# Performance work log

Measured on AMD Instinct MI355X. Metric: run time of the kernel, lower is better.

## Reference

```python
import jax, jax.numpy as jnp
import numpy as np

UNITS = 32
BACKBONE = 64

def lecun_tanh(x):
    return 1.7159 * jnp.tanh(0.666 * x)

def setup_inputs() -> dict:
    key = jax.random.key(0)
    ks = jax.random.split(key, 6)
    B, C, T, H, W = 4, 16, 32, 64, 64
    scale_b = 1.0 / np.sqrt(C + UNITS)
    scale_h = 1.0 / np.sqrt(BACKBONE)
    return {
        "x": jax.random.normal(ks[0], (B, C, T, H, W), jnp.float32),
        "Wb": jax.random.normal(ks[1], (BACKBONE, C + UNITS), jnp.float32) * scale_b,
        "bb": jnp.zeros((BACKBONE,), jnp.float32),
        "Wff1": jax.random.normal(ks[2], (UNITS, BACKBONE), jnp.float32) * scale_h,
        "bff1": jnp.zeros((UNITS,), jnp.float32),
        "Wff2": jax.random.normal(ks[3], (UNITS, BACKBONE), jnp.float32) * scale_h,
        "bff2": jnp.zeros((UNITS,), jnp.float32),
        "Wta": jax.random.normal(ks[4], (UNITS, BACKBONE), jnp.float32) * scale_h,
        "bta": jnp.zeros((UNITS,), jnp.float32),
        "Wtb": jax.random.normal(ks[5], (UNITS, BACKBONE), jnp.float32) * scale_h,
        "btb": jnp.zeros((UNITS,), jnp.float32),
    }

def reference(x, Wb, bb, Wff1, bff1, Wff2, bff2, Wta, bta, Wtb, btb):
    # x: (B, C, T, H, W) -> time-major (T, B, C, H, W) for the scan
    xs = jnp.transpose(x, (2, 0, 1, 3, 4))
    B, C, H, W = x.shape[0], x.shape[1], x.shape[3], x.shape[4]
    h0 = jnp.zeros((B, UNITS, H, W), x.dtype)
    ts = jnp.asarray(1.0, x.dtype)  # no timespans provided -> ts = 1.0

    def head(z, Wh, bh):  # channel-wise (1x1) linear: (B,K,H,W) -> (B,U,H,W)
        return jnp.einsum('bkhw,uk->buhw', z, Wh) + bh[None, :, None, None]

    def step(h, xt):
        z = jnp.concatenate([xt, h], axis=1)  # (B, C+U, H, W)
        z = lecun_tanh(jnp.einsum('bchw,kc->bkhw', z, Wb) + bb[None, :, None, None])
        ff1 = jnp.tanh(head(z, Wff1, bff1))
        ff2 = jnp.tanh(head(z, Wff2, bff2))
        t_a = head(z, Wta, bta)
        t_b = head(z, Wtb, btb)
        t_interp = jax.nn.sigmoid(t_a * ts + t_b)
        h_new = ff1 * (1.0 - t_interp) + t_interp * ff2
        return h_new, h_new

    _, ys = jax.lax.scan(step, h0, xs)  # ys: (T, B, U, H, W)
    # stack along dim=1 (batch_first) then permute(0,2,1,3,4) -> (B, U, T, H, W)
    return jnp.transpose(ys, (1, 2, 0, 3, 4))
```

## Files before the change

### kernel.cpp

```cpp
#include <hip/hip_runtime.h>
#include <hip/hip_bf16.h>


#define CIN      16
#define UNITS    32
#define BACKBONE 64
#define CZ       48
#define TSTEPS   32
#define HW       4096
#define NPIX     16
#define NTHREADS 256

typedef __attribute__((ext_vector_type(8))) short  short8;
typedef __attribute__((ext_vector_type(8))) __bf16 bf16x8;
typedef __attribute__((ext_vector_type(4))) float  float4v;
typedef __attribute__((ext_vector_type(4))) unsigned int uint4v;
typedef __attribute__((ext_vector_type(2))) unsigned int uint2v;

#define BAR_LDS() asm volatile("s_waitcnt lgkmcnt(0)\n\ts_barrier" ::: "memory")

__device__ __forceinline__ unsigned short bf16_rne(float f) {
    unsigned u = __float_as_uint(f);
    return (unsigned short)((u + 0x7FFFu + ((u >> 16) & 1u)) >> 16);
}
__device__ __forceinline__ float bf16_tof(unsigned short h) {
    return __uint_as_float(((unsigned)h) << 16);
}
__device__ __forceinline__ unsigned cvt_pk_bf16(float lo, float hi) {
    unsigned r;
    asm("v_cvt_pk_bf16_f32 %0, %1, %2" : "=v"(r) : "v"(lo), "v"(hi));
    return r;
}

#if __has_builtin(__builtin_amdgcn_exp2f)
#define EXP2F(x) __builtin_amdgcn_exp2f(x)
#else
#define EXP2F(x) __expf(0.69314718056f * (x))
#endif
#if __has_builtin(__builtin_amdgcn_rcpf)
#define RCPF(x) __builtin_amdgcn_rcpf(x)
#else
#define RCPF(x) __fdividef(1.0f, (x))
#endif

__device__ __forceinline__ float lecun_tanh_f(float v) {
    float e = EXP2F(1.92166925f * v);
    return fmaf(-3.4318f, RCPF(e + 1.0f), 1.7159f);
}
__device__ __forceinline__ float tanh_f(float v) {
    float e = EXP2F(2.88539008f * v);
    return fmaf(-2.0f, RCPF(e + 1.0f), 1.0f);
}
__device__ __forceinline__ float sigmoid_f(float v) {
    float e = EXP2F(-1.44269504f * v);
    return RCPF(1.0f + e);
}
__device__ __forceinline__ float4v mfma16(bf16x8 a, bf16x8 b, float4v c) {
    return __builtin_amdgcn_mfma_f32_16x16x32_bf16(a, b, c, 0, 0, 0);
}
__device__ __forceinline__ void split8(const float* v, bf16x8& hi, bf16x8& lo) {
    short8 sh, sl;
    #pragma unroll
    for (int j = 0; j < 8; ++j) {
        unsigned short h = bf16_rne(v[j]);
        sh[j] = (short)h;
        sl[j] = (short)bf16_rne(v[j] - bf16_tof(h));
    }
    hi = __builtin_bit_cast(bf16x8, sh);
    lo = __builtin_bit_cast(bf16x8, sl);
}
__device__ __forceinline__ bf16x8 pack8hi(const float* v) {
    short8 sh;
    #pragma unroll
    for (int j = 0; j < 8; ++j) sh[j] = (short)bf16_rne(v[j]);
    return __builtin_bit_cast(bf16x8, sh);
}

__global__ __launch_bounds__(NTHREADS, 4)
void cfc_mfma_kernel(const float* __restrict__ x,   const float* __restrict__ Wb,
                     const float* __restrict__ bb,
                     const float* __restrict__ Wff1, const float* __restrict__ bff1,
                     const float* __restrict__ Wff2, const float* __restrict__ bff2,
                     const float* __restrict__ Wta,  const float* __restrict__ bta,
                     const float* __restrict__ Wtb,  const float* __restrict__ btb,
                     float* __restrict__ out)
{
    __shared__ __align__(16) unsigned hbuf[2][64][2];
    __shared__ __align__(16) unsigned abuf[4][64][2];
    __shared__ __align__(16) unsigned xbuf[4][18][2];

    const int tid  = threadIdx.x;
    const int w    = tid >> 6;
    const int lane = tid & 63;
    const int ln   = lane & 15;
    const int lq   = lane >> 4;

    const int gpix = blockIdx.x * NPIX;
    const int b    = gpix >> 12;
    const int pinb = gpix & 4095;
    const int mt   = w;

    bf16x8 Whhi, Whlo;
    {
        float v[8];
        #pragma unroll
        for (int j = 0; j < 8; ++j)
            v[j] = Wb[(mt * 16 + ln) * CZ + CIN + lq * 8 + j];
        split8(v, Whhi, Whlo);
    }
    bf16x8 Wxhi, Wxlo;
    {
        float v[8];
        #pragma unroll
        for (int j = 0; j < 8; ++j)
            v[j] = (lq < 2) ? Wb[(mt * 16 + ln) * CZ + lq * 8 + j] : 0.0f;
        split8(v, Wxhi, Wxlo);
    }
    float4v BBv, Z4;
    #pragma unroll
    for (int r = 0; r < 4; ++r) { BBv[r] = bb[mt * 16 + lq * 4 + r]; Z4[r] = 0.0f; }

    const int head = ln & 3;
    const float* Whp = (head == 0) ? Wff1 : (head == 1) ? Wff2 : (head == 2) ? Wta : Wtb;
    const int urow = (ln >> 2) * 8;
    bf16x8 Ah[2][2];
    #pragma unroll
    for (int i2 = 0; i2 < 2; ++i2) {
        #pragma unroll
        for (int kt = 0; kt < 2; ++kt) {
            float v[8];
            #pragma unroll
            for (int j = 0; j < 8; ++j) {
                int n = 32 * kt + (j >> 2) * 16 + lq * 4 + (j & 3);
                v[j] = Whp[(urow + 2 * w + i2) * BACKBONE + n];
            }
            Ah[i2][kt] = pack8hi(v);
        }
    }
    const int ub = lq * 8;
    float4v HBv[2];
    #pragma unroll
    for (int i2 = 0; i2 < 2; ++i2) {
        int u2 = ub + 2 * w + i2;
        HBv[i2][0] = bff1[u2]; HBv[i2][1] = bff2[u2];
        HBv[i2][2] = bta[u2];  HBv[i2][3] = btb[u2];
    }

    const int  xr  = 2 * w + (lq & 1);
    const bool xpr = (lq < 2);
    const unsigned xi0 = ((unsigned)(b * CIN + 2 * xr) * TSTEPS) * HW
                         + (unsigned)(pinb + ln);
    const unsigned xi1 = xi0 + (unsigned)(TSTEPS * HW);

    const int r2base = (lq & 1) * 2;

    unsigned oo[2];
    #pragma unroll
    for (int i2 = 0; i2 < 2; ++i2)
        oo[i2] = ((unsigned)(b * UNITS + ub + 2 * w + i2) * TSTEPS) * HW
                 + (unsigned)(pinb + ln);

    auto xread = [&]() {
        uint2v x01 = *(const uint2v*)&xbuf[r2base][ln][0];
        uint2v x23 = *(const uint2v*)&xbuf[r2base + 1][ln][0];
        uint4v u = {x01[0], x01[1], x23[0], x23[1]};
        return u;
    };

    ((unsigned*)hbuf)[tid] = 0u;
    if (xpr) {
        float a0 = x[xi0], a1 = x[xi1];
        xbuf[xr >> 1][ln][xr & 1] = cvt_pk_bf16(a0, a1);
    }
    __syncthreads();
    float4v xzA, xzB;
    {
        uint4v u = xread();
        bf16x8 X0 = __builtin_bit_cast(bf16x8, u);
        float4v a = mfma16(Wxhi, X0, BBv);
        a = mfma16(Wxlo, X0, a);
        xzA = a;
    }
    __syncthreads();
    float pc0 = 0.f, pc1 = 0.f, pn0 = 0.f, pn1 = 0.f;
    if (xpr) {
        float a0 = x[xi0 + HW], a1 = x[xi1 + HW];
        xbuf[xr >> 1][ln][xr & 1] = cvt_pk_bf16(a0, a1);
        pc0 = x[xi0 + 2u * HW]; pc1 = x[xi1 + 2u * HW];
    }
    __syncthreads();
    unsigned toff = 0;

    __builtin_amdgcn_s_setprio(1);

    auto step = [&](int t, float4v xzc, float4v& xzn,
                    float& c0, float& c1, float& n0, float& n1) {
        const unsigned tl = (unsigned)((t + 3 < TSTEPS) ? t + 3 : TSTEPS - 1);
        if (xpr) { n0 = x[xi0 + tl * HW]; n1 = x[xi1 + tl * HW]; }

        uint4v xfu = xread();

        uint2v hA = *(const uint2v*)&hbuf[0][lane][0];
        uint2v hB = *(const uint2v*)&hbuf[1][lane][0];
        uint4v zv = {hA[0], hA[1], hB[0], hB[1]};
        bf16x8 Z = __builtin_bit_cast(bf16x8, zv);
        float4v ah = mfma16(Whhi, Z, xzc);
        float4v al = mfma16(Whlo, Z, Z4);
        float4v a  = ah + al;
        float g0 = lecun_tanh_f(a[0]);
        float g1 = lecun_tanh_f(a[1]);
        float g2 = lecun_tanh_f(a[2]);
        float g3 = lecun_tanh_f(a[3]);
        uint2v ad = {cvt_pk_bf16(g0, g1), cvt_pk_bf16(g2, g3)};
        *(uint2v*)&abuf[mt][lane][0] = ad;
        BAR_LDS();

        __builtin_amdgcn_s_setprio(0);
        if (xpr) xbuf[xr >> 1][ln][xr & 1] = cvt_pk_bf16(c0, c1);
        {
            bf16x8 X = __builtin_bit_cast(bf16x8, xfu);
            float4v q = mfma16(Wxhi, X, BBv);
            q = mfma16(Wxlo, X, q);
            xzn = q;
        }
        __builtin_amdgcn_s_setprio(1);

        uint2v a0 = *(const uint2v*)&abuf[0][lane][0];
        uint2v a1 = *(const uint2v*)&abuf[1][lane][0];
        uint2v a2 = *(const uint2v*)&abuf[2][lane][0];
        uint2v a3 = *(const uint2v*)&abuf[3][lane][0];
        uint4v w0 = {a0[0], a0[1], a1[0], a1[1]};
        uint4v w1 = {a2[0], a2[1], a3[0], a3[1]};
        bf16x8 A20 = __builtin_bit_cast(bf16x8, w0);
        bf16x8 A21 = __builtin_bit_cast(bf16x8, w1);

        float hn[2];
        #pragma unroll
        for (int i2 = 0; i2 < 2; ++i2) {
            float4v ch = mfma16(Ah[i2][0], A20, HBv[i2]);
            float4v cl = mfma16(Ah[i2][1], A21, Z4);
            float4v c  = ch + cl;
            float f1g = tanh_f(c[0]);
            float f2g = tanh_f(c[1]);
            float ti  = sigmoid_f(c[2] + c[3]);
            float h   = fmaf(ti, f2g - f1g, f1g);
            out[oo[i2] + toff] = h;
            hn[i2] = h;
        }
        hbuf[w >> 1][lane][w & 1] = cvt_pk_bf16(hn[0], hn[1]);
        BAR_LDS();
        toff += (unsigned)HW;
    };

    #pragma unroll 1
    for (int t = 0; t < TSTEPS; t += 2) {
        step(t,     xzA, xzB, pc0, pc1, pn0, pn1);
        step(t + 1, xzB, xzA, pn0, pn1, pc0, pc1);
    }
}

extern "C" void kernel_launch(void* const* d_in, const int* in_sizes, int n_in,
                              void* d_out, int out_size, void* d_ws, size_t ws_size,
                              hipStream_t stream) {
    dim3 grid(4 * HW / NPIX);
    cfc_mfma_kernel<<<grid, NTHREADS, 0, stream>>>(
        (const float*)d_in[0], (const float*)d_in[1], (const float*)d_in[2],
        (const float*)d_in[3], (const float*)d_in[4], (const float*)d_in[5],
        (const float*)d_in[6], (const float*)d_in[7], (const float*)d_in[8],
        (const float*)d_in[9], (const float*)d_in[10],
        (float*)d_out);
}
```

Baseline: 146.2 us.

## Halve threads per block, giving each wave two backbone tiles and four head rows

Cuts the block from 4 waves to 2. Each wave now computes two 16-row backbone MFMA tiles and four head output rows, and stages four x channels per lane. This halves the per-block barrier participants and spreads the same work over fewer waves. The cost is more serial MFMA and transcendental work per wave, more registers, and fewer waves per block to hide the recurrent step's latency.

```diff
diff --git a/kernel.cpp b/kernel.cpp
--- a/kernel.cpp
+++ b/kernel.cpp
@@ -9,7 +9,7 @@
 #define TSTEPS   32
 #define HW       4096
 #define NPIX     16
-#define NTHREADS 256
+#define NTHREADS 128
 
 typedef __attribute__((ext_vector_type(8))) short  short8;
 typedef __attribute__((ext_vector_type(8))) __bf16 bf16x8;
@@ -76,7 +76,7 @@
     return __builtin_bit_cast(bf16x8, sh);
 }
 
-__global__ __launch_bounds__(NTHREADS, 4)
+__global__ __launch_bounds__(NTHREADS, 2)
 void cfc_mfma_kernel(const float* __restrict__ x,   const float* __restrict__ Wb,
                      const float* __restrict__ bb,
                      const float* __restrict__ Wff1, const float* __restrict__ bff1,
@@ -98,66 +98,65 @@
     const int gpix = blockIdx.x * NPIX;
     const int b    = gpix >> 12;
     const int pinb = gpix & 4095;
-    const int mt   = w;
-
-    bf16x8 Whhi, Whlo;
-    {
+
+    bf16x8 Whhi[2], Whlo[2], Wxhi[2], Wxlo[2];
+    float4v BBv[2], Z4;
+    #pragma unroll
+    for (int r = 0; r < 4; ++r) Z4[r] = 0.0f;
+    #pragma unroll
+    for (int i = 0; i < 2; ++i) {
+        const int mt = 2 * w + i;
         float v[8];
         #pragma unroll
         for (int j = 0; j < 8; ++j)
             v[j] = Wb[(mt * 16 + ln) * CZ + CIN + lq * 8 + j];
-        split8(v, Whhi, Whlo);
-    }
-    bf16x8 Wxhi, Wxlo;
-    {
-        float v[8];
+        split8(v, Whhi[i], Whlo[i]);
         #pragma unroll
         for (int j = 0; j < 8; ++j)
             v[j] = (lq < 2) ? Wb[(mt * 16 + ln) * CZ + lq * 8 + j] : 0.0f;
-        split8(v, Wxhi, Wxlo);
-    }
-    float4v BBv, Z4;
-    #pragma unroll
-    for (int r = 0; r < 4; ++r) { BBv[r] = bb[mt * 16 + lq * 4 + r]; Z4[r] = 0.0f; }
+        split8(v, Wxhi[i], Wxlo[i]);
+        #pragma unroll
+        for (int r = 0; r < 4; ++r) BBv[i][r] = bb[mt * 16 + lq * 4 + r];
+    }
 
     const int head = ln & 3;
     const float* Whp = (head == 0) ? Wff1 : (head == 1) ? Wff2 : (head == 2) ? Wta : Wtb;
     const int urow = (ln >> 2) * 8;
-    bf16x8 Ah[2][2];
-    #pragma unroll
-    for (int i2 = 0; i2 < 2; ++i2) {
+    bf16x8 Ah[4][2];
+    float4v HBv[4];
+    const int ub = lq * 8;
+    #pragma unroll
+    for (int i2 = 0; i2 < 4; ++i2) {
+        const int ti = 4 * w + i2;
         #pragma unroll
         for (int kt = 0; kt < 2; ++kt) {
             float v[8];
             #pragma unroll
             for (int j = 0; j < 8; ++j) {
                 int n = 32 * kt + (j >> 2) * 16 + lq * 4 + (j & 3);
-                v[j] = Whp[(urow + 2 * w + i2) * BACKBONE + n];
+                v[j] = Whp[(urow + ti) * BACKBONE + n];
             }
             Ah[i2][kt] = pack8hi(v);
         }
-    }
-    const int ub = lq * 8;
-    float4v HBv[2];
-    #pragma unroll
-    for (int i2 = 0; i2 < 2; ++i2) {
-        int u2 = ub + 2 * w + i2;
+        int u2 = ub + ti;
         HBv[i2][0] = bff1[u2]; HBv[i2][1] = bff2[u2];
         HBv[i2][2] = bta[u2];  HBv[i2][3] = btb[u2];
     }
 
-    const int  xr  = 2 * w + (lq & 1);
     const bool xpr = (lq < 2);
-    const unsigned xi0 = ((unsigned)(b * CIN + 2 * xr) * TSTEPS) * HW
-                         + (unsigned)(pinb + ln);
-    const unsigned xi1 = xi0 + (unsigned)(TSTEPS * HW);
+    const int  xrow2 = 2 * w + (lq & 1);
+    const int  chb   = 8 * w + 4 * (lq & 1);
+    unsigned xi[4];
+    #pragma unroll
+    for (int k = 0; k < 4; ++k)
+        xi[k] = ((unsigned)(b * CIN + chb + k) * TSTEPS) * HW + (unsigned)(pinb + ln);
 
     const int r2base = (lq & 1) * 2;
 
-    unsigned oo[2];
-    #pragma unroll
-    for (int i2 = 0; i2 < 2; ++i2)
-        oo[i2] = ((unsigned)(b * UNITS + ub + 2 * w + i2) * TSTEPS) * HW
+    unsigned oo[4];
+    #pragma unroll
+    for (int i2 = 0; i2 < 4; ++i2)
+        oo[i2] = ((unsigned)(b * UNITS + ub + 4 * w + i2) * TSTEPS) * HW
                  + (unsigned)(pinb + ln);
 
     auto xread = [&]() {
@@ -166,62 +165,83 @@
         uint4v u = {x01[0], x01[1], x23[0], x23[1]};
         return u;
     };
+    auto xstage = [&](const float (&v)[4]) {
+        uint2v d = {cvt_pk_bf16(v[0], v[1]), cvt_pk_bf16(v[2], v[3])};
+        *(uint2v*)&xbuf[xrow2][ln][0] = d;
+    };
 
     ((unsigned*)hbuf)[tid] = 0u;
+    ((unsigned*)hbuf)[tid + 128] = 0u;
+    float pc[4] = {0, 0, 0, 0}, pn[4] = {0, 0, 0, 0};
     if (xpr) {
-        float a0 = x[xi0], a1 = x[xi1];
-        xbuf[xr >> 1][ln][xr & 1] = cvt_pk_bf16(a0, a1);
+        float v0[4];
+        #pragma unroll
+        for (int k = 0; k < 4; ++k) v0[k] = x[xi[k]];
+        xstage(v0);
     }
     __syncthreads();
-    float4v xzA, xzB;
+    float4v xzA[2], xzB[2];
     {
         uint4v u = xread();
         bf16x8 X0 = __builtin_bit_cast(bf16x8, u);
-        float4v a = mfma16(Wxhi, X0, BBv);
-        a = mfma16(Wxlo, X0, a);
-        xzA = a;
+        #pragma unroll
+        for (int i = 0; i < 2; ++i) {
+            float4v a = mfma16(Wxhi[i], X0, BBv[i]);
+            a = mfma16(Wxlo[i], X0, a);
+            xzA[i] = a;
+        }
     }
     __syncthreads();
-    float pc0 = 0.f, pc1 = 0.f, pn0 = 0.f, pn1 = 0.f;
     if (xpr) {
-        float a0 = x[xi0 + HW], a1 = x[xi1 + HW];
-        xbuf[xr >> 1][ln][xr & 1] = cvt_pk_bf16(a0, a1);
-        pc0 = x[xi0 + 2u * HW]; pc1 = x[xi1 + 2u * HW];
+        float v1[4];
+        #pragma unroll
+        for (int k = 0; k < 4; ++k) v1[k] = x[xi[k] + HW];
+        xstage(v1);
+        #pragma unroll
+        for (int k = 0; k < 4; ++k) pc[k] = x[xi[k] + 2u * HW];
     }
     __syncthreads();
     unsigned toff = 0;
 
     __builtin_amdgcn_s_setprio(1);
 
-    auto step = [&](int t, float4v xzc, float4v& xzn,
-                    float& c0, float& c1, float& n0, float& n1) {
+    auto step = [&](int t, float4v (&xzc)[2], float4v (&xzn)[2],
+                    float (&c)[4], float (&n)[4]) {
         const unsigned tl = (unsigned)((t + 3 < TSTEPS) ? t + 3 : TSTEPS - 1);
-        if (xpr) { n0 = x[xi0 + tl * HW]; n1 = x[xi1 + tl * HW]; }
-
+        if (xpr) {
+            #pragma unroll
+            for (int k = 0; k < 4; ++k) n[k] = x[xi[k] + tl * HW];
+        }
         uint4v xfu = xread();
 
         uint2v hA = *(const uint2v*)&hbuf[0][lane][0];
         uint2v hB = *(const uint2v*)&hbuf[1][lane][0];
         uint4v zv = {hA[0], hA[1], hB[0], hB[1]};
         bf16x8 Z = __builtin_bit_cast(bf16x8, zv);
-        float4v ah = mfma16(Whhi, Z, xzc);
-        float4v al = mfma16(Whlo, Z, Z4);
-        float4v a  = ah + al;
-        float g0 = lecun_tanh_f(a[0]);
-        float g1 = lecun_tanh_f(a[1]);
-        float g2 = lecun_tanh_f(a[2]);
-        float g3 = lecun_tanh_f(a[3]);
-        uint2v ad = {cvt_pk_bf16(g0, g1), cvt_pk_bf16(g2, g3)};
-        *(uint2v*)&abuf[mt][lane][0] = ad;
+        #pragma unroll
+        for (int i = 0; i < 2; ++i) {
+            float4v ah = mfma16(Whhi[i], Z, xzc[i]);
+            float4v al = mfma16(Whlo[i], Z, Z4);
+            float4v a  = ah + al;
+            float g0 = lecun_tanh_f(a[0]);
+            float g1 = lecun_tanh_f(a[1]);
+            float g2 = lecun_tanh_f(a[2]);
+            float g3 = lecun_tanh_f(a[3]);
+            uint2v ad = {cvt_pk_bf16(g0, g1), cvt_pk_bf16(g2, g3)};
+            *(uint2v*)&abuf[2 * w + i][lane][0] = ad;
+        }
         BAR_LDS();
 
         __builtin_amdgcn_s_setprio(0);
-        if (xpr) xbuf[xr >> 1][ln][xr & 1] = cvt_pk_bf16(c0, c1);
+        if (xpr) xstage(c);
         {
             bf16x8 X = __builtin_bit_cast(bf16x8, xfu);
-            float4v q = mfma16(Wxhi, X, BBv);
-            q = mfma16(Wxlo, X, q);
-            xzn = q;
+            #pragma unroll
+            for (int i = 0; i < 2; ++i) {
+                float4v q = mfma16(Wxhi[i], X, BBv[i]);
+                q = mfma16(Wxlo[i], X, q);
+                xzn[i] = q;
+            }
         }
         __builtin_amdgcn_s_setprio(1);
 
@@ -234,28 +254,29 @@
         bf16x8 A20 = __builtin_bit_cast(bf16x8, w0);
         bf16x8 A21 = __builtin_bit_cast(bf16x8, w1);
 
-        float hn[2];
-        #pragma unroll
-        for (int i2 = 0; i2 < 2; ++i2) {
+        float hn[4];
+        #pragma unroll
+        for (int i2 = 0; i2 < 4; ++i2) {
             float4v ch = mfma16(Ah[i2][0], A20, HBv[i2]);
             float4v cl = mfma16(Ah[i2][1], A21, Z4);
-            float4v c  = ch + cl;
-            float f1g = tanh_f(c[0]);
-            float f2g = tanh_f(c[1]);
-            float ti  = sigmoid_f(c[2] + c[3]);
+            float4v cc = ch + cl;
+            float f1g = tanh_f(cc[0]);
+            float f2g = tanh_f(cc[1]);
+            float ti  = sigmoid_f(cc[2] + cc[3]);
             float h   = fmaf(ti, f2g - f1g, f1g);
             out[oo[i2] + toff] = h;
             hn[i2] = h;
         }
-        hbuf[w >> 1][lane][w & 1] = cvt_pk_bf16(hn[0], hn[1]);
+        uint2v hd = {cvt_pk_bf16(hn[0], hn[1]), cvt_pk_bf16(hn[2], hn[3])};
+        *(uint2v*)&hbuf[w][lane][0] = hd;
         BAR_LDS();
         toff += (unsigned)HW;
     };
 
     #pragma unroll 1
     for (int t = 0; t < TSTEPS; t += 2) {
-        step(t,     xzA, xzB, pc0, pc1, pn0, pn1);
-        step(t + 1, xzB, xzA, pn0, pn1, pc0, pc1);
+        step(t,     xzA, xzB, pc, pn);
+        step(t + 1, xzB, xzA, pn, pc);
     }
 }
 
```

Result: no change. 145.5 us (-0.5%).
